# Kernel tuning notes

Measured on AMD Instinct MI355X. Metric: run time of the kernel, lower is better.

The kernel has to match this reference:

```python
import jax, jax.numpy as jnp
import numpy as np

B, SE, SD, IN_DIM, D, DEPTH, H, DH, M, FF, NBINS = 8, 2048, 1024, 1280, 512, 4, 8, 64, 266, 2048, 128

def _ln(x, g, b):
    mu = x.mean(-1, keepdims=True)
    var = ((x - mu) ** 2).mean(-1, keepdims=True)
    return (x - mu) / jnp.sqrt(var + 1e-5) * g + b

def _gelu(x):
    return jax.nn.gelu(x, approximate=False)

def _sinusoidal(x, dim):
    # sinusoidal embedding of integer expression bins -> [.., dim]
    half = dim // 2
    freqs = jnp.exp(-jnp.log(10000.0) * jnp.arange(half, dtype=jnp.float32) / half)
    ang = x[..., None].astype(jnp.float32) * freqs
    return jnp.concatenate([jnp.sin(ang), jnp.cos(ang)], axis=-1)

def _split_heads(x):
    b, s, _ = x.shape
    return x.reshape(b, s, H, DH).transpose(0, 2, 1, 3)

def _merge_heads(x):
    b, h, s, d = x.shape
    return x.transpose(0, 2, 1, 3).reshape(b, s, h * d)

def _favor_attention(q, k, v, proj):
    # FAVOR+ softmax-kernel linear attention (non-causal), performer-style
    dn = DH ** -0.25
    ratio = M ** -0.5
    eps = 1e-4
    qd = jnp.einsum('bhsd,md->bhsm', q * dn, proj)
    kd = jnp.einsum('bhsd,md->bhsm', k * dn, proj)
    q_diag = 0.5 * (q ** 2).sum(-1, keepdims=True) * dn * dn
    k_diag = 0.5 * (k ** 2).sum(-1, keepdims=True) * dn * dn
    qp = ratio * (jnp.exp(qd - q_diag - jnp.max(qd, axis=-1, keepdims=True)) + eps)
    kp = ratio * (jnp.exp(kd - k_diag - jnp.max(kd)) + eps)
    k_sum = kp.sum(axis=2)                                   # [b,h,m]
    d_inv = 1.0 / jnp.einsum('bhsm,bhm->bhs', qp, k_sum)     # [b,h,s]
    kv = jnp.einsum('bhsm,bhsd->bhmd', kp, v)                # [b,h,m,d]
    return jnp.einsum('bhsm,bhmd->bhsd', qp, kv) * d_inv[..., None]

def _forward(var_input_encoder, var_input_decoder, var_W, var_b, enc_ln_g, enc_ln_b, dec_ln_g, dec_ln_b, p_ln1_g, p_ln1_b, p_Wq, p_Wk, p_Wv, p_Wo, p_bo, p_ln2_g, p_ln2_b, p_w1, p_b1, p_w2, p_b2, proj, ca_Wq, ca_Wk, ca_Wv, ca_Wo, ca_bo, cross_ln_g, cross_ln_b, ffd_w1, ffd_b1, ffd_w2, ffd_b2, out_ln_g, out_ln_b, head_W, head_b, expression_encoder):
    expr = _sinusoidal(expression_encoder, D)            # [B,SE,D]
    enc = var_input_encoder @ var_W + var_b              # [B,SE,D]
    dec = var_input_decoder @ var_W + var_b              # [B,SD,D]
    x = _ln(enc + expr, enc_ln_g, enc_ln_b)
    # Performer encoder: pre-LN self-attn (FAVOR+) + pre-LN FF, residuals
    for i in range(DEPTH):
        y = _ln(x, p_ln1_g[i], p_ln1_b[i])
        q = _split_heads(y @ p_Wq[i])
        k = _split_heads(y @ p_Wk[i])
        v = _split_heads(y @ p_Wv[i])
        x = x + (_merge_heads(_favor_attention(q, k, v, proj[i])) @ p_Wo[i] + p_bo[i])
        y = _ln(x, p_ln2_g[i], p_ln2_b[i])
        x = x + (_gelu(y @ p_w1[i] + p_b1[i]) @ p_w2[i] + p_b2[i])
    context = x
    # decoder: LN -> softmax cross-attention over encoder context
    dec = _ln(dec, dec_ln_g, dec_ln_b)
    q = _split_heads(dec @ ca_Wq)
    k = _split_heads(context @ ca_Wk)
    v = _split_heads(context @ ca_Wv)
    scores = jnp.einsum('bhqd,bhkd->bhqk', q, k) * (DH ** -0.5)
    o = _merge_heads(jnp.einsum('bhqk,bhkd->bhqd', jax.nn.softmax(scores, axis=-1), v)) @ ca_Wo + ca_bo
    out = _ln(o + dec, cross_ln_g, cross_ln_b)
    out = _gelu(out @ ffd_w1 + ffd_b1) @ ffd_w2 + ffd_b2   # note: no residual around FF (as in source)
    out = _ln(out, out_ln_g, out_ln_b)
    return out @ head_W + head_b                            # [B,SD,NBINS]

def setup_inputs() -> dict:
    key = jax.random.key(0)
    ks = iter(jax.random.split(key, 64))
    def w(shape, scale=0.02):
        return jax.random.normal(next(ks), shape, dtype=jnp.float32) * scale
    inp = {
        'var_input_encoder': jax.random.normal(next(ks), (B, SE, IN_DIM), dtype=jnp.float32),
        'var_input_decoder': jax.random.normal(next(ks), (B, SD, IN_DIM), dtype=jnp.float32),
        'expression_encoder': jax.random.randint(next(ks), (B, SE), 0, NBINS, dtype=jnp.int32),
        'var_W': w((IN_DIM, D)), 'var_b': jnp.zeros((D,), jnp.float32),
        'enc_ln_g': jnp.ones((D,), jnp.float32), 'enc_ln_b': jnp.zeros((D,), jnp.float32),
        'dec_ln_g': jnp.ones((D,), jnp.float32), 'dec_ln_b': jnp.zeros((D,), jnp.float32),
        'p_ln1_g': jnp.ones((DEPTH, D), jnp.float32), 'p_ln1_b': jnp.zeros((DEPTH, D), jnp.float32),
        'p_Wq': w((DEPTH, D, H * DH)), 'p_Wk': w((DEPTH, D, H * DH)), 'p_Wv': w((DEPTH, D, H * DH)),
        'p_Wo': w((DEPTH, H * DH, D)), 'p_bo': jnp.zeros((DEPTH, D), jnp.float32),
        'p_ln2_g': jnp.ones((DEPTH, D), jnp.float32), 'p_ln2_b': jnp.zeros((DEPTH, D), jnp.float32),
        'p_w1': w((DEPTH, D, FF)), 'p_b1': jnp.zeros((DEPTH, FF), jnp.float32),
        'p_w2': w((DEPTH, FF, D)), 'p_b2': jnp.zeros((DEPTH, D), jnp.float32),
        'proj': jax.random.normal(next(ks), (DEPTH, M, DH), dtype=jnp.float32),
        'ca_Wq': w((D, H * DH)), 'ca_Wk': w((D, H * DH)), 'ca_Wv': w((D, H * DH)),
        'ca_Wo': w((H * DH, D)), 'ca_bo': jnp.zeros((D,), jnp.float32),
        'cross_ln_g': jnp.ones((D,), jnp.float32), 'cross_ln_b': jnp.zeros((D,), jnp.float32),
        'ffd_w1': w((D, FF)), 'ffd_b1': jnp.zeros((FF,), jnp.float32),
        'ffd_w2': w((FF, D)), 'ffd_b2': jnp.zeros((D,), jnp.float32),
        'out_ln_g': jnp.ones((D,), jnp.float32), 'out_ln_b': jnp.zeros((D,), jnp.float32),
        'head_W': w((D, NBINS)), 'head_b': jnp.zeros((NBINS,), jnp.float32),
    }
    return inp

def reference(var_input_encoder, var_input_decoder, expression_encoder, var_W, var_b, enc_ln_g, enc_ln_b, dec_ln_g, dec_ln_b, p_ln1_g, p_ln1_b, p_Wq, p_Wk, p_Wv, p_Wo, p_bo, p_ln2_g, p_ln2_b, p_w1, p_b1, p_w2, p_b2, proj, ca_Wq, ca_Wk, ca_Wv, ca_Wo, ca_bo, cross_ln_g, cross_ln_b, ffd_w1, ffd_b1, ffd_w2, ffd_b2, out_ln_g, out_ln_b, head_W, head_b):
    return _forward(var_input_encoder, var_input_decoder, var_W, var_b, enc_ln_g, enc_ln_b, dec_ln_g, dec_ln_b, p_ln1_g, p_ln1_b, p_Wq, p_Wk, p_Wv, p_Wo, p_bo, p_ln2_g, p_ln2_b, p_w1, p_b1, p_w2, p_b2, proj, ca_Wq, ca_Wk, ca_Wv, ca_Wo, ca_bo, cross_ln_g, cross_ln_b, ffd_w1, ffd_b1, ffd_w2, ffd_b2, out_ln_g, out_ln_b, head_W, head_b, expression_encoder)
```

## Files before the change

### kernel.cpp

```cpp
#include <hip/hip_runtime.h>
#include <hip/hip_bf16.h>
#include <math.h>

constexpr int cB = 8, cSE = 2048, cSD = 1024, cIN = 1280, cD = 512,
              cDEPTH = 4, cH = 8, cDH = 64, cM = 266, cFF = 2048, cNB = 128;
constexpr int cMP = 288;

#define DEV __device__ __forceinline__

typedef __bf16 bf16;
typedef __attribute__((ext_vector_type(8))) __bf16 bf16x8;
typedef __attribute__((ext_vector_type(4))) __bf16 bf16x4;
typedef __attribute__((ext_vector_type(2))) __bf16 bf16x2;
typedef __attribute__((ext_vector_type(4))) float f32x4;

DEV float gelu_f(float x) { return 0.5f * x * (1.0f + erff(x * 0.70710678118654752440f)); }

DEV float wave_sum(float v) {
#pragma unroll
  for (int o = 32; o; o >>= 1) v += __shfl_xor(v, o);
  return v;
}
DEV float wave_max(float v) {
#pragma unroll
  for (int o = 32; o; o >>= 1) v = fmaxf(v, __shfl_xor(v, o));
  return v;
}

#define GL2LDS(gp, lp) __builtin_amdgcn_global_load_lds(                    \
    (const __attribute__((address_space(1))) void*)(gp),                    \
    (__attribute__((address_space(3))) void*)(lp), 16, 0, 0)

template <int OUT, int ACT, bool BIAS, bool RES>
__global__ __launch_bounds__(256) void gemm_mfma(
    const bf16* __restrict__ A, const bf16* __restrict__ Bt,
    void* __restrict__ Cv, bf16* __restrict__ Cv2,
    const float* __restrict__ bias, int M, int N, int K) {
  __shared__ bf16 As[128 * 32];
  __shared__ bf16 Bs[128 * 32];
  const int t = threadIdx.x, l = t & 63, w = t >> 6;
  const int g = l >> 4, c = l & 15;
  const int nwg = gridDim.x * gridDim.y;
  int id = blockIdx.y * gridDim.x + blockIdx.x;
  if ((nwg & 7) == 0) id = (id & 7) * (nwg >> 3) + (id >> 3);
  const int m0 = (id / gridDim.x) * 128, n0 = (id % gridDim.x) * 128;
  const int wr = (w >> 1) * 64, wc = (w & 1) * 64;
  const int srow = w * 32 + (l >> 2);
  const int scol = (l & 3) * 8;
  const bf16* gA = A + (size_t)(m0 + srow) * K + scol;
  const bf16* gB = Bt + (size_t)(n0 + srow) * K + scol;
  bf16* lA = As + w * 1024;
  bf16* lB = Bs + w * 1024;

  const f32x4 zero4 = {0.f, 0.f, 0.f, 0.f};
  f32x4 acc[4][4];
#pragma unroll
  for (int i = 0; i < 4; i++)
#pragma unroll
    for (int j = 0; j < 4; j++) acc[i][j] = zero4;

  for (int k0 = 0; k0 < K; k0 += 32) {
    GL2LDS(gA + k0, lA);
    GL2LDS(gA + (size_t)16 * K + k0, lA + 512);
    GL2LDS(gB + k0, lB);
    GL2LDS(gB + (size_t)16 * K + k0, lB + 512);
    __syncthreads();
    bf16x8 af[4], bfr[4];
#pragma unroll
    for (int i = 0; i < 4; i++)
      af[i] = *(const bf16x8*)(As + (wr + i * 16 + c) * 32 + g * 8);
#pragma unroll
    for (int j = 0; j < 4; j++)
      bfr[j] = *(const bf16x8*)(Bs + (wc + j * 16 + c) * 32 + g * 8);
#pragma unroll
    for (int i = 0; i < 4; i++)
#pragma unroll
      for (int j = 0; j < 4; j++)
        acc[i][j] = __builtin_amdgcn_mfma_f32_16x16x32_bf16(af[i], bfr[j], acc[i][j], 0, 0, 0);
    __syncthreads();
  }
  float* Cf = (float*)Cv;
  bf16* Cb = (bf16*)Cv;
#pragma unroll
  for (int i = 0; i < 4; i++) {
    const int mb = m0 + wr + i * 16 + g * 4;
#pragma unroll
    for (int j = 0; j < 4; j++) {
      const int n = n0 + wc + j * 16 + c;
      const float bv = BIAS ? bias[n] : 0.f;
#pragma unroll
      for (int r = 0; r < 4; r++) {
        float v = acc[i][j][r] + bv;
        if (ACT == 1) v = gelu_f(v);
        const size_t idx = (size_t)(mb + r) * N + n;
        if (OUT == 0 || OUT == 2) {
          float* cp = Cf + idx;
          if (RES) v += *cp;
          *cp = v;
          if (OUT == 2) Cv2[idx] = (bf16)v;
        } else {
          Cb[idx] = (bf16)v;
        }
      }
    }
  }
}

__global__ __launch_bounds__(256) void transpose_cast(
    const float* __restrict__ W, bf16* __restrict__ Wt, int K, int N) {
  __shared__ float tile[32][33];
  const int tx = threadIdx.x & 31, ty = threadIdx.x >> 5;
  const int k0 = blockIdx.y * 32, n0 = blockIdx.x * 32;
#pragma unroll
  for (int i = ty; i < 32; i += 8) tile[i][tx] = W[(size_t)(k0 + i) * N + n0 + tx];
  __syncthreads();
#pragma unroll
  for (int i = ty; i < 32; i += 8)
    Wt[(size_t)(n0 + i) * K + k0 + tx] = (bf16)tile[tx][i];
}

__global__ __launch_bounds__(256) void transpose_cast4(
    const float* __restrict__ W0, const float* __restrict__ W1,
    const float* __restrict__ W2, const float* __restrict__ W3,
    bf16* __restrict__ Wt) {
  __shared__ float tile[32][33];
  const int zz = blockIdx.z;
  const float* W = zz == 0 ? W0 : zz == 1 ? W1 : zz == 2 ? W2 : W3;
  bf16* dst = Wt + (size_t)zz * 262144;
  const int tx = threadIdx.x & 31, ty = threadIdx.x >> 5;
  const int k0 = blockIdx.y * 32, n0 = blockIdx.x * 32;
#pragma unroll
  for (int i = ty; i < 32; i += 8) tile[i][tx] = W[(size_t)(k0 + i) * 512 + n0 + tx];
  __syncthreads();
#pragma unroll
  for (int i = ty; i < 32; i += 8)
    dst[(size_t)(n0 + i) * 512 + k0 + tx] = (bf16)tile[tx][i];
}

__global__ __launch_bounds__(256) void transpose_castFF(
    const float* __restrict__ w1s, const float* __restrict__ w2s,
    bf16* __restrict__ d1, bf16* __restrict__ d2) {
  __shared__ float tile[32][33];
  const int z = blockIdx.y;
  const int K = z ? 2048 : 512, N = z ? 512 : 2048;
  const float* W = z ? w2s : w1s;
  bf16* dst = z ? d2 : d1;
  const int nt = N >> 5;
  const int bid = blockIdx.x;
  const int n0 = (bid % nt) * 32, k0 = (bid / nt) * 32;
  const int tx = threadIdx.x & 31, ty = threadIdx.x >> 5;
#pragma unroll
  for (int i = ty; i < 32; i += 8) tile[i][tx] = W[(size_t)(k0 + i) * N + n0 + tx];
  __syncthreads();
#pragma unroll
  for (int i = ty; i < 32; i += 8)
    dst[(size_t)(n0 + i) * K + k0 + tx] = (bf16)tile[tx][i];
}

__global__ __launch_bounds__(256) void castf2b(
    const float* __restrict__ x, bf16* __restrict__ y, int n) {
  int i = (blockIdx.x * 256 + threadIdx.x) * 4;
  const int stride = gridDim.x * 1024;
  for (; i < n; i += stride) {
    float4 v = *(const float4*)(x + i);
    bf16x4 o;
    o[0] = (bf16)v.x; o[1] = (bf16)v.y; o[2] = (bf16)v.z; o[3] = (bf16)v.w;
    *(bf16x4*)(y + i) = o;
  }
}

__global__ __launch_bounds__(256) void proj_cast(
    const float* __restrict__ proj, bf16* __restrict__ projB) {
  const int idx = blockIdx.x * 256 + threadIdx.x;
  if (idx >= cMP * cDH) return;
  const int m = idx >> 6;
  projB[idx] = (bf16)(m < cM ? proj[idx] * 0.35355339059327373f : 0.f);
}

__global__ __launch_bounds__(256) void vtrans(
    const bf16* __restrict__ Vh, int ld, bf16* __restrict__ Vt) {
  __shared__ bf16 tile[64][65];
  const int z = blockIdx.y, b = z >> 3, h = z & 7;
  const int s0 = blockIdx.x * 64;
  const int t = threadIdx.x;
#pragma unroll
  for (int r = t >> 3; r < 64; r += 32) {
    bf16x8 v = *(const bf16x8*)(Vh + ((size_t)b * cSE + s0 + r) * ld + h * cDH + (t & 7) * 8);
#pragma unroll
    for (int e = 0; e < 8; e++) tile[(t & 7) * 8 + e][r] = v[e];
  }
  __syncthreads();
  bf16* vz = Vt + (size_t)z * 80 * cSE;
#pragma unroll
  for (int d = t >> 3; d < 64; d += 32) {
    bf16x8 o;
#pragma unroll
    for (int e = 0; e < 8; e++) o[e] = tile[d][(t & 7) * 8 + e];
    *(bf16x8*)(vz + (size_t)d * cSE + s0 + (t & 7) * 8) = o;
  }
  const int rr = t >> 4, seg = (t & 15) * 4;
  bf16x4 ov;
  const float val = (rr == 0) ? 1.f : 0.f;
  ov[0] = (bf16)val; ov[1] = (bf16)val; ov[2] = (bf16)val; ov[3] = (bf16)val;
  *(bf16x4*)(vz + (size_t)(64 + rr) * cSE + s0 + seg) = ov;
}

template <int MODE>
__global__ __launch_bounds__(256, 1) void favor_phik(
    const bf16* __restrict__ Kh, int ld, const bf16* __restrict__ projB,
    float* __restrict__ bmax, bf16* __restrict__ Pout) {
  __shared__ float sm[4];
  const int z = blockIdx.y, b = z >> 3, h = z & 7;
  const int s0 = blockIdx.x * 128;
  const int t = threadIdx.x, l = t & 63, w = t >> 6, g = l >> 4, c = l & 15;
  const int wr = (w >> 1) * 64, wcol = (w & 1) * 144;

  float gm = 0.f;
  if (MODE == 2) {
    float m = -1e30f;
    for (int i = t; i < 1024; i += 256) m = fmaxf(m, bmax[i]);
    m = wave_max(m);
    if (l == 0) sm[w] = m;
    __syncthreads();
    gm = fmaxf(fmaxf(sm[0], sm[1]), fmaxf(sm[2], sm[3]));
  }

  const f32x4 zero4 = {0.f, 0.f, 0.f, 0.f};
  f32x4 acc[4][9];
#pragma unroll
  for (int i = 0; i < 4; i++)
#pragma unroll
    for (int j = 0; j < 9; j++) acc[i][j] = zero4;
  float sq[4] = {0.f, 0.f, 0.f, 0.f};
  const size_t abase = ((size_t)b * cSE + s0) * ld + h * cDH;
#pragma unroll
  for (int k0 = 0; k0 < 64; k0 += 32) {
    bf16x8 af[4];
#pragma unroll
    for (int i = 0; i < 4; i++) {
      af[i] = *(const bf16x8*)(Kh + abase + (size_t)(wr + i * 16 + c) * ld + k0 + g * 8);
      if (MODE == 2) {
#pragma unroll
        for (int e = 0; e < 8; e++) {
          const float v = (float)af[i][e];
          sq[i] += v * v;
        }
      }
    }
#pragma unroll
    for (int j = 0; j < 9; j++) {
      bf16x8 bfr = *(const bf16x8*)(projB + (wcol + j * 16 + c) * 64 + k0 + g * 8);
#pragma unroll
      for (int i = 0; i < 4; i++)
        acc[i][j] = __builtin_amdgcn_mfma_f32_16x16x32_bf16(af[i], bfr, acc[i][j], 0, 0, 0);
    }
  }
  const float ratio = 0.061313927f;

  if (MODE == 1) {
    float m = -3e38f;
#pragma unroll
    for (int i = 0; i < 4; i++)
#pragma unroll
      for (int j = 0; j < 9; j++) {
        const int mc = wcol + j * 16 + c;
        if (mc < cM) {
#pragma unroll
          for (int r = 0; r < 4; r++) m = fmaxf(m, acc[i][j][r]);
        }
      }
    m = wave_max(m);
    if (l == 0) sm[w] = m;
    __syncthreads();
    if (t == 0)
      bmax[blockIdx.y * 16 + blockIdx.x] =
          fmaxf(fmaxf(sm[0], sm[1]), fmaxf(sm[2], sm[3]));
    return;
  }

#pragma unroll
  for (int i = 0; i < 4; i++) {
    sq[i] += __shfl_xor(sq[i], 16);
    sq[i] += __shfl_xor(sq[i], 32);
  }
  float rowsub[4][4];
#pragma unroll
  for (int i = 0; i < 4; i++)
#pragma unroll
    for (int r = 0; r < 4; r++)
      rowsub[i][r] = gm + 0.0625f * __shfl(sq[i], g * 4 + r);

#pragma unroll
  for (int i = 0; i < 4; i++)
#pragma unroll
    for (int j = 0; j < 9; j++) {
      const int mc = wcol + j * 16 + c;
      bf16x4 o;
#pragma unroll
      for (int r = 0; r < 4; r++) {
        const float v = (mc < cM)
            ? ratio * (__expf(acc[i][j][r] - rowsub[i][r]) + 1e-4f) : 0.f;
        o[r] = (bf16)v;
      }
      *(bf16x4*)(Pout + ((size_t)z * cMP + mc) * cSE + s0 + wr + i * 16 + g * 4) = o;
    }
}

__global__ __launch_bounds__(256) void favor_kv(
    const bf16* __restrict__ Pk, const bf16* __restrict__ Vt,
    float* __restrict__ part) {
  const int z = blockIdx.y, ch = blockIdx.x;
  const int t = threadIdx.x, l = t & 63, w = t >> 6, g = l >> 4, c = l & 15;
  const int wm = (w & 1) * 144, wd = (w >> 1) * 32;
  const bool dden = (wd == 32);
  const size_t pkz = (size_t)z * cMP * cSE, vtz = (size_t)z * 80 * cSE;
  const f32x4 zero4 = {0.f, 0.f, 0.f, 0.f};
  f32x4 acc[9][2], accx[9];
#pragma unroll
  for (int j = 0; j < 9; j++) {
    acc[j][0] = zero4; acc[j][1] = zero4; accx[j] = zero4;
  }
  for (int k0 = ch * 512; k0 < ch * 512 + 512; k0 += 32) {
    bf16x8 bv[2], bvx;
#pragma unroll
    for (int i = 0; i < 2; i++)
      bv[i] = *(const bf16x8*)(Vt + vtz + (size_t)(wd + i * 16 + c) * cSE + k0 + g * 8);
    if (dden)
      bvx = *(const bf16x8*)(Vt + vtz + (size_t)(64 + c) * cSE + k0 + g * 8);
#pragma unroll
    for (int j = 0; j < 9; j++) {
      bf16x8 am = *(const bf16x8*)(Pk + pkz + (size_t)(wm + j * 16 + c) * cSE + k0 + g * 8);
      acc[j][0] = __builtin_amdgcn_mfma_f32_16x16x32_bf16(am, bv[0], acc[j][0], 0, 0, 0);
      acc[j][1] = __builtin_amdgcn_mfma_f32_16x16x32_bf16(am, bv[1], acc[j][1], 0, 0, 0);
      if (dden)
        accx[j] = __builtin_amdgcn_mfma_f32_16x16x32_bf16(am, bvx, accx[j], 0, 0, 0);
    }
  }
  float* po = part + ((size_t)z * 4 + ch) * (cMP * 80);
#pragma unroll
  for (int j = 0; j < 9; j++)
#pragma unroll
    for (int i = 0; i < 2; i++)
#pragma unroll
      for (int r = 0; r < 4; r++)
        po[(size_t)(wm + j * 16 + g * 4 + r) * 80 + wd + i * 16 + c] = acc[j][i][r];
  if (dden) {
#pragma unroll
    for (int j = 0; j < 9; j++)
#pragma unroll
      for (int r = 0; r < 4; r++)
        po[(size_t)(wm + j * 16 + g * 4 + r) * 80 + 64 + c] = accx[j][r];
  }
}

__global__ __launch_bounds__(256) void kv_reduce(
    const float* __restrict__ part, bf16* __restrict__ kvT) {
  const int z = blockIdx.x;
  const float* p = part + (size_t)z * 4 * (cMP * 80);
  bf16* o = kvT + (size_t)z * 80 * cMP;
  for (int idx = threadIdx.x; idx < cMP * 80; idx += 256) {
    const int m = idx / 80, d = idx - m * 80;
    const float s = p[idx] + p[idx + cMP * 80] + p[idx + 2 * cMP * 80] + p[idx + 3 * cMP * 80];
    o[(size_t)d * cMP + m] = (bf16)s;
  }
}

__global__ __launch_bounds__(256, 1) void favor_qout(
    const bf16* __restrict__ Qh, int ld, const bf16* __restrict__ projB,
    const bf16* __restrict__ kvT, bf16* __restrict__ Y) {
  __shared__ bf16 Plds[128 * 296];
  __shared__ float rmaxs[4][64];
  __shared__ float denl[128];
  const int z = blockIdx.y, b = z >> 3, h = z & 7;
  const int s0 = blockIdx.x * 128;
  const int t = threadIdx.x, l = t & 63, w = t >> 6, g = l >> 4, c = l & 15;
  const int wr = (w >> 1) * 64, wcol = (w & 1) * 144;
  const f32x4 zero4 = {0.f, 0.f, 0.f, 0.f};
  f32x4 acc[4][9];
#pragma unroll
  for (int i = 0; i < 4; i++)
#pragma unroll
    for (int j = 0; j < 9; j++) acc[i][j] = zero4;
  float sq[4] = {0.f, 0.f, 0.f, 0.f};
  const size_t abase = ((size_t)b * cSE + s0) * ld + h * cDH;
#pragma unroll
  for (int k0 = 0; k0 < 64; k0 += 32) {
    bf16x8 af[4];
#pragma unroll
    for (int i = 0; i < 4; i++) {
      af[i] = *(const bf16x8*)(Qh + abase + (size_t)(wr + i * 16 + c) * ld + k0 + g * 8);
#pragma unroll
      for (int e = 0; e < 8; e++) {
        const float v = (float)af[i][e];
        sq[i] += v * v;
      }
    }
#pragma unroll
    for (int j = 0; j < 9; j++) {
      bf16x8 bfr = *(const bf16x8*)(projB + (wcol + j * 16 + c) * 64 + k0 + g * 8);
#pragma unroll
      for (int i = 0; i < 4; i++)
        acc[i][j] = __builtin_amdgcn_mfma_f32_16x16x32_bf16(af[i], bfr, acc[i][j], 0, 0, 0);
    }
  }
#pragma unroll
  for (int i = 0; i < 4; i++) {
    sq[i] += __shfl_xor(sq[i], 16);
    sq[i] += __shfl_xor(sq[i], 32);
  }
  const float ratio = 0.061313927f;
  float rowsub[4][4];
#pragma unroll
  for (int i = 0; i < 4; i++)
#pragma unroll
    for (int r = 0; r < 4; r++) {
      float m = -3e38f;
#pragma unroll
      for (int j = 0; j < 9; j++) {
        const int mc = wcol + j * 16 + c;
        m = (mc < cM) ? fmaxf(m, acc[i][j][r]) : m;
      }
      m = fmaxf(m, __shfl_xor(m, 1));
      m = fmaxf(m, __shfl_xor(m, 2));
      m = fmaxf(m, __shfl_xor(m, 4));
      m = fmaxf(m, __shfl_xor(m, 8));
      rowsub[i][r] = m;
    }
  if (c == 0) {
#pragma unroll
    for (int i = 0; i < 4; i++)
#pragma unroll
      for (int r = 0; r < 4; r++) rmaxs[w][i * 16 + g * 4 + r] = rowsub[i][r];
  }
  __syncthreads();
#pragma unroll
  for (int i = 0; i < 4; i++)
#pragma unroll
    for (int r = 0; r < 4; r++) {
      const int row = i * 16 + g * 4 + r;
      rowsub[i][r] = fmaxf(rowsub[i][r], rmaxs[w ^ 1][row]) +
                     0.0625f * __shfl(sq[i], g * 4 + r);
    }
#pragma unroll
  for (int i = 0; i < 4; i++)
#pragma unroll
    for (int j = 0; j < 9; j++) {
      const int mc = wcol + j * 16 + c;
#pragma unroll
      for (int r = 0; r < 4; r++) {
        const float v = (mc < cM)
            ? ratio * (__expf(acc[i][j][r] - rowsub[i][r]) + 1e-4f) : 0.f;
        Plds[(wr + i * 16 + g * 4 + r) * 296 + mc] = (bf16)v;
      }
    }
  __syncthreads();

  const int wd = (w & 1) * 32;
  const bool dden = (wd == 32);
  f32x4 acc2[4][2], accx[4];
#pragma unroll
  for (int i = 0; i < 4; i++) {
    acc2[i][0] = zero4; acc2[i][1] = zero4; accx[i] = zero4;
  }
  const size_t kz = (size_t)z * 80 * cMP;
#pragma unroll 3
  for (int k0 = 0; k0 < cMP; k0 += 32) {
    bf16x8 bv[2], bvx;
#pragma unroll
    for (int j = 0; j < 2; j++)
      bv[j] = *(const bf16x8*)(kvT + kz + (size_t)(wd + j * 16 + c) * cMP + k0 + g * 8);
    if (dden)
      bvx = *(const bf16x8*)(kvT + kz + (size_t)(64 + c) * cMP + k0 + g * 8);
#pragma unroll
    for (int i = 0; i < 4; i++) {
      bf16x8 av = *(const bf16x8*)(Plds + (wr + i * 16 + c) * 296 + k0 + g * 8);
      acc2[i][0] = __builtin_amdgcn_mfma_f32_16x16x32_bf16(av, bv[0], acc2[i][0], 0, 0, 0);
      acc2[i][1] = __builtin_amdgcn_mfma_f32_16x16x32_bf16(av, bv[1], acc2[i][1], 0, 0, 0);
      if (dden)
        accx[i] = __builtin_amdgcn_mfma_f32_16x16x32_bf16(av, bvx, accx[i], 0, 0, 0);
    }
  }
  if (dden && c == 0) {
#pragma unroll
    for (int i = 0; i < 4; i++)
#pragma unroll
      for (int r = 0; r < 4; r++)
        denl[wr + i * 16 + g * 4 + r] = accx[i][r];
  }
  __syncthreads();
#pragma unroll
  for (int i = 0; i < 4; i++)
#pragma unroll
    for (int r = 0; r < 4; r++) {
      const int row = wr + i * 16 + g * 4 + r;
      const float inv = 1.0f / denl[row];
#pragma unroll
      for (int j = 0; j < 2; j++)
        Y[((size_t)b * cSE + s0 + row) * cD + h * cDH + wd + j * 16 + c] =
            (bf16)(acc2[i][j][r] * inv);
    }
}

template <bool ADD, bool WF, bool WB>
__global__ __launch_bounds__(256) void ln_rows(
    const float* __restrict__ in, const float* __restrict__ add,
    const float* __restrict__ g, const float* __restrict__ be,
    float* __restrict__ out, bf16* __restrict__ out2) {
  const int wid = blockIdx.x * 4 + (threadIdx.x >> 6);
  const int lane = threadIdx.x & 63;
  const float* ip = in + (size_t)wid * cD + lane * 8;
  float x[8];
  {
    float4 a = *(const float4*)ip;
    float4 b4 = *(const float4*)(ip + 4);
    x[0] = a.x; x[1] = a.y; x[2] = a.z; x[3] = a.w;
    x[4] = b4.x; x[5] = b4.y; x[6] = b4.z; x[7] = b4.w;
  }
  if (ADD) {
    const float* ap = add + (size_t)wid * cD + lane * 8;
    float4 a = *(const float4*)ap;
    float4 b4 = *(const float4*)(ap + 4);
    x[0] += a.x; x[1] += a.y; x[2] += a.z; x[3] += a.w;
    x[4] += b4.x; x[5] += b4.y; x[6] += b4.z; x[7] += b4.w;
  }
  float s = 0;
#pragma unroll
  for (int i = 0; i < 8; i++) s += x[i];
  s = wave_sum(s);
  const float mu = s * (1.0f / cD);
  float vs = 0;
#pragma unroll
  for (int i = 0; i < 8; i++) { const float d = x[i] - mu; vs += d * d; }
  vs = wave_sum(vs);
  const float rstd = 1.0f / sqrtf(vs * (1.0f / cD) + 1e-5f);
  float r[8];
#pragma unroll
  for (int i = 0; i < 8; i++) {
    const int d = lane * 8 + i;
    r[i] = (x[i] - mu) * rstd * g[d] + be[d];
  }
  if (WF) {
    float* op = out + (size_t)wid * cD + lane * 8;
    float4 a, b4;
    a.x = r[0]; a.y = r[1]; a.z = r[2]; a.w = r[3];
    b4.x = r[4]; b4.y = r[5]; b4.z = r[6]; b4.w = r[7];
    *(float4*)op = a; *(float4*)(op + 4) = b4;
  }
  if (WB) {
    bf16x8 ov;
#pragma unroll
    for (int i = 0; i < 8; i++) ov[i] = (bf16)r[i];
    *(bf16x8*)(out2 + (size_t)wid * cD + lane * 8) = ov;
  }
}

__global__ __launch_bounds__(256) void embed_ln(
    float* __restrict__ X, const int* __restrict__ ids,
    const float* __restrict__ g, const float* __restrict__ be) {
  const int wid = blockIdx.x * 4 + (threadIdx.x >> 6);
  const int lane = threadIdx.x & 63;
  const float idv = (float)ids[wid];
  float* xp = X + (size_t)wid * cD + lane * 8;
  float x[8];
  {
    float4 a = *(const float4*)xp;
    float4 b4 = *(const float4*)(xp + 4);
    x[0] = a.x; x[1] = a.y; x[2] = a.z; x[3] = a.w;
    x[4] = b4.x; x[5] = b4.y; x[6] = b4.z; x[7] = b4.w;
  }
  const float kf = -0.03597789207803197f;
#pragma unroll
  for (int i = 0; i < 8; i++) {
    const int d = lane * 8 + i;
    float e;
    if (d < 256) e = sinf(idv * expf(kf * (float)d));
    else         e = cosf(idv * expf(kf * (float)(d - 256)));
    x[i] += e;
  }
  float s = 0;
#pragma unroll
  for (int i = 0; i < 8; i++) s += x[i];
  s = wave_sum(s);
  const float mu = s * (1.0f / cD);
  float vs = 0;
#pragma unroll
  for (int i = 0; i < 8; i++) { const float d = x[i] - mu; vs += d * d; }
  vs = wave_sum(vs);
  const float rstd = 1.0f / sqrtf(vs * (1.0f / cD) + 1e-5f);
#pragma unroll
  for (int i = 0; i < 8; i++) {
    const int d = lane * 8 + i;
    xp[i] = (x[i] - mu) * rstd * g[d] + be[d];
  }
}

__global__ __launch_bounds__(256) void flash_mfma(
    const bf16* __restrict__ Q, const bf16* __restrict__ Kc,
    const bf16* __restrict__ Vc, bf16* __restrict__ O, int ldkv) {
  __shared__ __align__(16) bf16 KP[4 * 16 * 136];
  __shared__ __align__(16) bf16 Vs[80 * 136];
  const int id = blockIdx.x;
  const int b = (id & 63) >> 3, h = id & 7, qb = id >> 6;
  const int t = threadIdx.x, l = t & 63, w = t >> 6, g = l >> 4, c = l & 15;
  const int q0 = qb * 64 + w * 16;
  bf16x8 aq[2];
  {
    const bf16* qp = Q + ((size_t)b * cSD + q0 + c) * cD + h * cDH + g * 8;
    aq[0] = *(const bf16x8*)qp;
    aq[1] = *(const bf16x8*)(qp + 32);
  }
  for (int idx = t; idx < 16 * 136; idx += 256) {
    const int rr = idx / 136, cc = idx - rr * 136;
    Vs[(64 + rr) * 136 + cc] = (bf16)(rr == 0 ? 1.f : 0.f);
  }
  const f32x4 zero4 = {0.f, 0.f, 0.f, 0.f};
  f32x4 o5[5];
#pragma unroll
  for (int j = 0; j < 5; j++) o5[j] = zero4;
  float mrow[4];
#pragma unroll
  for (int r = 0; r < 4; r++) mrow[r] = -1e30f;

  const int kr = t >> 1, kof = (t & 1) * 32;
  const int sidx = t & 31, dseg = t >> 5;
  const size_t kvbase = (size_t)b * cSE * ldkv + h * cDH;
  char* KsC = (char*)KP;
  bf16* Pw = KP + w * 16 * 136;
  const float S2 = 0.18033688011112042f;
  const float T2 = 11.541560327111708f;

  bf16x8 pk[4], pv[4];
  auto LOADR = [&](int kt) {
    const bf16* kp = Kc + kvbase + (size_t)(kt + kr) * ldkv + kof;
#pragma unroll
    for (int i = 0; i < 4; i++) pk[i] = *(const bf16x8*)(kp + i * 8);
    const bf16* vp = Vc + kvbase + (size_t)(kt + 4 * sidx) * ldkv + dseg * 8;
#pragma unroll
    for (int i = 0; i < 4; i++) pv[i] = *(const bf16x8*)(vp + (size_t)i * ldkv);
  };
  auto WRITEL = [&]() {
    const int sw = (kr & 7) << 4;
#pragma unroll
    for (int i = 0; i < 4; i++)
      *(bf16x8*)(KsC + kr * 128 + (((kof + i * 8) * 2) ^ sw)) = pk[i];
#pragma unroll
    for (int e = 0; e < 8; e++) {
      bf16x4 q4;
      q4[0] = pv[0][e]; q4[1] = pv[1][e]; q4[2] = pv[2][e]; q4[3] = pv[3][e];
      *(bf16x4*)(Vs + (dseg * 8 + e) * 136 + 4 * sidx) = q4;
    }
  };
  LOADR(0);
  WRITEL();

  for (int kt = 0; kt < cSE; kt += 128) {
    const bool more = (kt + 128 < cSE);
    if (more) LOADR(kt + 128);
    __syncthreads();
    f32x4 s4[8];
#pragma unroll
    for (int t2 = 0; t2 < 8; t2++) {
      const int kr2 = t2 * 16 + c;
      const int sw2 = (kr2 & 7) << 4;
      bf16x8 bk0 = *(const bf16x8*)(KsC + kr2 * 128 + ((g * 16) ^ sw2));
      bf16x8 bk1 = *(const bf16x8*)(KsC + kr2 * 128 + ((64 + g * 16) ^ sw2));
      f32x4 z = zero4;
      z = __builtin_amdgcn_mfma_f32_16x16x32_bf16(aq[0], bk0, z, 0, 0, 0);
      z = __builtin_amdgcn_mfma_f32_16x16x32_bf16(aq[1], bk1, z, 0, 0, 0);
      s4[t2] = z;
    }
    __syncthreads();
#pragma unroll
    for (int r = 0; r < 4; r++) {
      float xv[8];
#pragma unroll
      for (int t2 = 0; t2 < 8; t2++) xv[t2] = s4[t2][r] * S2;
      float tm = xv[0];
#pragma unroll
      for (int t2 = 1; t2 < 8; t2++) tm = fmaxf(tm, xv[t2]);
      tm = fmaxf(tm, __shfl_xor(tm, 1));
      tm = fmaxf(tm, __shfl_xor(tm, 2));
      tm = fmaxf(tm, __shfl_xor(tm, 4));
      tm = fmaxf(tm, __shfl_xor(tm, 8));
      if (tm > mrow[r] + T2) {
        const float corr = exp2f(mrow[r] - tm);
        mrow[r] = tm;
#pragma unroll
        for (int j = 0; j < 5; j++) o5[j][r] *= corr;
      }
      const float m = mrow[r];
      const int qr = g * 4 + r;
#pragma unroll
      for (int t2 = 0; t2 < 8; t2++)
        Pw[qr * 136 + t2 * 16 + c] = (bf16)exp2f(xv[t2] - m);
    }
    bf16x8 pa[4];
#pragma unroll
    for (int ks = 0; ks < 4; ks++)
      pa[ks] = *(const bf16x8*)(Pw + c * 136 + ks * 32 + g * 8);
#pragma unroll
    for (int j = 0; j < 5; j++) {
#pragma unroll
      for (int ks = 0; ks < 4; ks++) {
        bf16x8 bv = *(const bf16x8*)(Vs + (j * 16 + c) * 136 + ks * 32 + g * 8);
        o5[j] = __builtin_amdgcn_mfma_f32_16x16x32_bf16(pa[ks], bv, o5[j], 0, 0, 0);
      }
    }
    __syncthreads();
    if (more) WRITEL();
  }
#pragma unroll
  for (int r = 0; r < 4; r++) {
    const float den = __shfl(o5[4][r], l & 48);
    const float inv = 1.0f / den;
    const size_t row = (size_t)b * cSD + q0 + g * 4 + r;
#pragma unroll
    for (int j = 0; j < 4; j++)
      O[row * cD + h * cDH + j * 16 + c] = (bf16)(o5[j][r] * inv);
  }
}

extern "C" void kernel_launch(void* const* d_in, const int* in_sizes, int n_in,
                              void* d_out, int out_size, void* d_ws, size_t ws_size,
                              hipStream_t stream) {
  const float* in_enc = (const float*)d_in[0];
  const float* in_dec = (const float*)d_in[1];
  const int* expr = (const int*)d_in[2];
  const float* var_W = (const float*)d_in[3];
  const float* var_b = (const float*)d_in[4];
  const float* enc_g = (const float*)d_in[5];
  const float* enc_b = (const float*)d_in[6];
  const float* dec_g = (const float*)d_in[7];
  const float* dec_b = (const float*)d_in[8];
  const float* ln1_g = (const float*)d_in[9];
  const float* ln1_b = (const float*)d_in[10];
  const float* Wq = (const float*)d_in[11];
  const float* Wk = (const float*)d_in[12];
  const float* Wv = (const float*)d_in[13];
  const float* Wo = (const float*)d_in[14];
  const float* bo = (const float*)d_in[15];
  const float* ln2_g = (const float*)d_in[16];
  const float* ln2_b = (const float*)d_in[17];
  const float* w1 = (const float*)d_in[18];
  const float* b1 = (const float*)d_in[19];
  const float* w2 = (const float*)d_in[20];
  const float* b2 = (const float*)d_in[21];
  const float* proj = (const float*)d_in[22];
  const float* caWq = (const float*)d_in[23];
  const float* caWk = (const float*)d_in[24];
  const float* caWv = (const float*)d_in[25];
  const float* caWo = (const float*)d_in[26];
  const float* cabo = (const float*)d_in[27];
  const float* crg = (const float*)d_in[28];
  const float* crb = (const float*)d_in[29];
  const float* fw1 = (const float*)d_in[30];
  const float* fb1 = (const float*)d_in[31];
  const float* fw2 = (const float*)d_in[32];
  const float* fb2 = (const float*)d_in[33];
  const float* og = (const float*)d_in[34];
  const float* ob = (const float*)d_in[35];
  const float* hW = (const float*)d_in[36];
  const float* hb = (const float*)d_in[37];

  float* X     = (float*)d_ws;
  float* DC    = X + 8388608;
  bf16*  QKV   = (bf16*)(DC + 4194304);
  bf16*  Vt    = QKV + 25165824;
  bf16*  Pq    = Vt + 10485760;
  bf16*  Pk    = Pq + 37748736;
  float* part  = (float*)(Pk + 37748736);
  bf16*  kvT   = (bf16*)(part + 5898240);
  float* bmax  = (float*)(kvT + 1474560);
  bf16*  Yb    = (bf16*)(bmax + 1040);
  bf16*  DCb   = Yb + 8388608;
  bf16*  Wt    = DCb + 4194304;
  bf16*  projB = Wt + 1048576;
  bf16*  Wt2   = projB + 18432;
  const size_t need_bytes = (size_t)82143264 * 4;
  if (ws_size < need_bytes) return;

  bf16* Pb   = Pq;
  bf16* encB = Pb;
  bf16* decB = Pk;
  bf16* Pmid = Pb;
  bf16* Xb   = Vt;
  bf16* Qc   = Pb + 8388608;
  bf16* KVc  = Pb + 12582912;
  bf16* Fb   = Pb + 29360128;
  bf16* Pm2  = Pb + 33554432;

  const dim3 blk(256);

  castf2b<<<2048, blk, 0, stream>>>(in_enc, encB, 16384 * 1280);
  castf2b<<<2048, blk, 0, stream>>>(in_dec, decB, 8192 * 1280);
  transpose_cast<<<dim3(16, 40), blk, 0, stream>>>(var_W, Wt, 1280, 512);
  gemm_mfma<0, 0, true, false><<<dim3(4, 128), blk, 0, stream>>>(encB, Wt, X, nullptr, var_b, 16384, 512, 1280);
  gemm_mfma<0, 0, true, false><<<dim3(4, 64), blk, 0, stream>>>(decB, Wt, DC, nullptr, var_b, 8192, 512, 1280);
  embed_ln<<<4096, blk, 0, stream>>>(X, expr, enc_g, enc_b);
  ln_rows<false, true, true><<<2048, blk, 0, stream>>>(DC, nullptr, dec_g, dec_b, DC, DCb);

  for (int i = 0; i < cDEPTH; i++) {
    ln_rows<false, false, true><<<4096, blk, 0, stream>>>(X, nullptr, ln1_g + i * cD, ln1_b + i * cD, nullptr, Yb);
    transpose_cast4<<<dim3(16, 16, 4), blk, 0, stream>>>(
        Wq + (size_t)i * cD * cD, Wk + (size_t)i * cD * cD,
        Wv + (size_t)i * cD * cD, Wo + (size_t)i * cD * cD, Wt);
    gemm_mfma<1, 0, false, false><<<dim3(12, 128), blk, 0, stream>>>(Yb, Wt, QKV, nullptr, nullptr, 16384, 1536, 512);
    proj_cast<<<72, blk, 0, stream>>>(proj + (size_t)i * cM * cDH, projB);
    vtrans<<<dim3(32, 64), blk, 0, stream>>>(QKV + 1024, 1536, Vt);
    favor_phik<1><<<dim3(16, 64), blk, 0, stream>>>(QKV + 512, 1536, projB, bmax, nullptr);
    favor_phik<2><<<dim3(16, 64), blk, 0, stream>>>(QKV + 512, 1536, projB, bmax, Pk);
    favor_kv<<<dim3(4, 64), blk, 0, stream>>>(Pk, Vt, part);
    kv_reduce<<<64, blk, 0, stream>>>(part, kvT);
    favor_qout<<<dim3(16, 64), blk, 0, stream>>>(QKV, 1536, projB, kvT, Yb);
    gemm_mfma<0, 0, true, true><<<dim3(4, 128), blk, 0, stream>>>(Yb, Wt + 786432, X, nullptr, bo + i * cD, 16384, 512, 512);
    ln_rows<false, false, true><<<4096, blk, 0, stream>>>(X, nullptr, ln2_g + i * cD, ln2_b + i * cD, nullptr, Yb);
    transpose_castFF<<<dim3(1024, 2), blk, 0, stream>>>(
        w1 + (size_t)i * cD * cFF, w2 + (size_t)i * cFF * cD, Wt, Wt2);
    gemm_mfma<1, 1, true, false><<<dim3(16, 128), blk, 0, stream>>>(Yb, Wt, Pmid, nullptr, b1 + i * cFF, 16384, 2048, 512);
    if (i < cDEPTH - 1) {
      gemm_mfma<0, 0, true, true><<<dim3(4, 128), blk, 0, stream>>>(Pmid, Wt2, X, nullptr, b2 + i * cD, 16384, 512, 2048);
    } else {
      gemm_mfma<2, 0, true, true><<<dim3(4, 128), blk, 0, stream>>>(Pmid, Wt2, X, Xb, b2 + i * cD, 16384, 512, 2048);
    }
  }

  transpose_cast4<<<dim3(16, 16, 4), blk, 0, stream>>>(caWq, caWk, caWv, caWo, Wt);
  gemm_mfma<1, 0, false, false><<<dim3(4, 64), blk, 0, stream>>>(DCb, Wt, Qc, nullptr, nullptr, 8192, 512, 512);
  gemm_mfma<1, 0, false, false><<<dim3(8, 128), blk, 0, stream>>>(Xb, Wt + 262144, KVc, nullptr, nullptr, 16384, 1024, 512);
  flash_mfma<<<dim3(1024), blk, 0, stream>>>(Qc, KVc, KVc + 512, Fb, 1024);
  gemm_mfma<0, 0, true, false><<<dim3(4, 64), blk, 0, stream>>>(Fb, Wt + 786432, X, nullptr, cabo, 8192, 512, 512);
  ln_rows<true, false, true><<<2048, blk, 0, stream>>>(X, DC, crg, crb, nullptr, Yb);
  transpose_castFF<<<dim3(1024, 2), blk, 0, stream>>>(fw1, fw2, Wt, Wt2);
  gemm_mfma<1, 1, true, false><<<dim3(16, 64), blk, 0, stream>>>(Yb, Wt, Pm2, nullptr, fb1, 8192, 2048, 512);
  gemm_mfma<0, 0, true, false><<<dim3(4, 64), blk, 0, stream>>>(Pm2, Wt2, X + 4194304, nullptr, fb2, 8192, 512, 2048);
  ln_rows<false, false, true><<<2048, blk, 0, stream>>>(X + 4194304, nullptr, og, ob, nullptr, Yb);
  transpose_cast<<<dim3(4, 16), blk, 0, stream>>>(hW, Wt, 512, 128);
  gemm_mfma<0, 0, true, false><<<dim3(1, 64), blk, 0, stream>>>(Yb, Wt, (float*)d_out, nullptr, hb, 8192, 128, 512);
}
```

Baseline: 2.276 ms.

## Fuse FAVOR key feature map with KV accumulation via shared memory

Merges the second key feature-map pass and the KV contraction into a single kernel. Each block computes exp feature tiles for 64 keys into LDS and immediately multiplies them with V, so the large Pk buffer is never written to or read from global memory. The work is split into 8 sequence chunks instead of 4, and kv_reduce now sums 8 partials. Separately, the softmax scale of the cross-attention query is folded into the Q projection GEMM epilogue, removing a multiply in the flash loop. The fused kernel keeps many accumulators live, which adds register pressure, and it needs extra block barriers.

```diff
diff --git a/kernel.cpp b/kernel.cpp
--- a/kernel.cpp
+++ b/kernel.cpp
@@ -92,6 +92,7 @@
       for (int r = 0; r < 4; r++) {
         float v = acc[i][j][r] + bv;
         if (ACT == 1) v = gelu_f(v);
+        if (ACT == 2) v *= 0.18033688011112042f;
         const size_t idx = (size_t)(mb + r) * N + n;
         if (OUT == 0 || OUT == 2) {
           float* cp = Cf + idx;
@@ -205,18 +206,65 @@
   *(bf16x4*)(vz + (size_t)(64 + rr) * cSE + s0 + seg) = ov;
 }
 
-template <int MODE>
-__global__ __launch_bounds__(256, 1) void favor_phik(
+__global__ __launch_bounds__(256, 1) void favor_kmax(
     const bf16* __restrict__ Kh, int ld, const bf16* __restrict__ projB,
-    float* __restrict__ bmax, bf16* __restrict__ Pout) {
+    float* __restrict__ bmax) {
   __shared__ float sm[4];
   const int z = blockIdx.y, b = z >> 3, h = z & 7;
   const int s0 = blockIdx.x * 128;
   const int t = threadIdx.x, l = t & 63, w = t >> 6, g = l >> 4, c = l & 15;
   const int wr = (w >> 1) * 64, wcol = (w & 1) * 144;
-
-  float gm = 0.f;
-  if (MODE == 2) {
+  const f32x4 zero4 = {0.f, 0.f, 0.f, 0.f};
+  f32x4 acc[4][9];
+#pragma unroll
+  for (int i = 0; i < 4; i++)
+#pragma unroll
+    for (int j = 0; j < 9; j++) acc[i][j] = zero4;
+  const size_t abase = ((size_t)b * cSE + s0) * ld + h * cDH;
+#pragma unroll
+  for (int k0 = 0; k0 < 64; k0 += 32) {
+    bf16x8 af[4];
+#pragma unroll
+    for (int i = 0; i < 4; i++)
+      af[i] = *(const bf16x8*)(Kh + abase + (size_t)(wr + i * 16 + c) * ld + k0 + g * 8);
+#pragma unroll
+    for (int j = 0; j < 9; j++) {
+      bf16x8 bfr = *(const bf16x8*)(projB + (wcol + j * 16 + c) * 64 + k0 + g * 8);
+#pragma unroll
+      for (int i = 0; i < 4; i++)
+        acc[i][j] = __builtin_amdgcn_mfma_f32_16x16x32_bf16(af[i], bfr, acc[i][j], 0, 0, 0);
+    }
+  }
+  float m = -3e38f;
+#pragma unroll
+  for (int i = 0; i < 4; i++)
+#pragma unroll
+    for (int j = 0; j < 9; j++) {
+      const int mc = wcol + j * 16 + c;
+      if (mc < cM) {
+#pragma unroll
+        for (int r = 0; r < 4; r++) m = fmaxf(m, acc[i][j][r]);
+      }
+    }
+  m = wave_max(m);
+  if (l == 0) sm[w] = m;
+  __syncthreads();
+  if (t == 0)
+    bmax[blockIdx.y * 16 + blockIdx.x] =
+        fmaxf(fmaxf(sm[0], sm[1]), fmaxf(sm[2], sm[3]));
+}
+
+__global__ __launch_bounds__(256, 1) void favor_kkv(
+    const bf16* __restrict__ Kh, int ld, const bf16* __restrict__ projB,
+    const bf16* __restrict__ Vt, const float* __restrict__ bmax,
+    float* __restrict__ part) {
+  __shared__ bf16 kp[288 * 72];
+  __shared__ float sm[4];
+  const int z = blockIdx.y, b = z >> 3, h = z & 7;
+  const int chunk = blockIdx.x;
+  const int t = threadIdx.x, l = t & 63, w = t >> 6, g = l >> 4, c = l & 15;
+  float gm;
+  {
     float m = -1e30f;
     for (int i = t; i < 1024; i += 256) m = fmaxf(m, bmax[i]);
     m = wave_max(m);
@@ -224,143 +272,118 @@
     __syncthreads();
     gm = fmaxf(fmaxf(sm[0], sm[1]), fmaxf(sm[2], sm[3]));
   }
-
+  const int pr = (w >> 1) * 32;
+  const int wcol = (w & 1) * 144;
+  const int wm = (w & 1) * 144, wd = (w >> 1) * 32;
+  const bool dden = (wd == 32);
+  const float ratio = 0.061313927f;
   const f32x4 zero4 = {0.f, 0.f, 0.f, 0.f};
-  f32x4 acc[4][9];
-#pragma unroll
-  for (int i = 0; i < 4; i++)
-#pragma unroll
-    for (int j = 0; j < 9; j++) acc[i][j] = zero4;
-  float sq[4] = {0.f, 0.f, 0.f, 0.f};
-  const size_t abase = ((size_t)b * cSE + s0) * ld + h * cDH;
-#pragma unroll
-  for (int k0 = 0; k0 < 64; k0 += 32) {
-    bf16x8 af[4];
-#pragma unroll
-    for (int i = 0; i < 4; i++) {
-      af[i] = *(const bf16x8*)(Kh + abase + (size_t)(wr + i * 16 + c) * ld + k0 + g * 8);
-      if (MODE == 2) {
+  f32x4 kacc[9][2], kaccx[9];
+#pragma unroll
+  for (int j = 0; j < 9; j++) {
+    kacc[j][0] = zero4; kacc[j][1] = zero4; kaccx[j] = zero4;
+  }
+  const size_t kbase = (size_t)b * cSE * ld + h * cDH;
+  const size_t vtz = (size_t)z * 80 * cSE;
+
+  for (int st = 0; st < 256; st += 64) {
+    const int sg = chunk * 256 + st;
+    f32x4 pacc[2][9];
+#pragma unroll
+    for (int i = 0; i < 2; i++)
+#pragma unroll
+      for (int j = 0; j < 9; j++) pacc[i][j] = zero4;
+    float sq[2] = {0.f, 0.f};
+#pragma unroll
+    for (int k0 = 0; k0 < 64; k0 += 32) {
+      bf16x8 af[2];
+#pragma unroll
+      for (int i = 0; i < 2; i++) {
+        af[i] = *(const bf16x8*)(Kh + kbase + (size_t)(sg + pr + i * 16 + c) * ld + k0 + g * 8);
 #pragma unroll
         for (int e = 0; e < 8; e++) {
           const float v = (float)af[i][e];
           sq[i] += v * v;
         }
       }
-    }
-#pragma unroll
-    for (int j = 0; j < 9; j++) {
-      bf16x8 bfr = *(const bf16x8*)(projB + (wcol + j * 16 + c) * 64 + k0 + g * 8);
-#pragma unroll
-      for (int i = 0; i < 4; i++)
-        acc[i][j] = __builtin_amdgcn_mfma_f32_16x16x32_bf16(af[i], bfr, acc[i][j], 0, 0, 0);
-    }
-  }
-  const float ratio = 0.061313927f;
-
-  if (MODE == 1) {
-    float m = -3e38f;
-#pragma unroll
-    for (int i = 0; i < 4; i++)
+#pragma unroll
+      for (int j = 0; j < 9; j++) {
+        bf16x8 bfr = *(const bf16x8*)(projB + (wcol + j * 16 + c) * 64 + k0 + g * 8);
+        pacc[0][j] = __builtin_amdgcn_mfma_f32_16x16x32_bf16(af[0], bfr, pacc[0][j], 0, 0, 0);
+        pacc[1][j] = __builtin_amdgcn_mfma_f32_16x16x32_bf16(af[1], bfr, pacc[1][j], 0, 0, 0);
+      }
+    }
+#pragma unroll
+    for (int i = 0; i < 2; i++) {
+      sq[i] += __shfl_xor(sq[i], 16);
+      sq[i] += __shfl_xor(sq[i], 32);
+    }
+    float rowsub[2][4];
+#pragma unroll
+    for (int i = 0; i < 2; i++)
+#pragma unroll
+      for (int r = 0; r < 4; r++)
+        rowsub[i][r] = gm + 0.0625f * __shfl(sq[i], g * 4 + r);
+    __syncthreads();
+#pragma unroll
+    for (int i = 0; i < 2; i++)
 #pragma unroll
       for (int j = 0; j < 9; j++) {
         const int mc = wcol + j * 16 + c;
-        if (mc < cM) {
-#pragma unroll
-          for (int r = 0; r < 4; r++) m = fmaxf(m, acc[i][j][r]);
+        bf16x4 o;
+#pragma unroll
+        for (int r = 0; r < 4; r++) {
+          const float v = (mc < cM)
+              ? ratio * (__expf(pacc[i][j][r] - rowsub[i][r]) + 1e-4f) : 0.f;
+          o[r] = (bf16)v;
         }
-      }
-    m = wave_max(m);
-    if (l == 0) sm[w] = m;
+        *(bf16x4*)(kp + (size_t)mc * 72 + pr + i * 16 + g * 4) = o;
+      }
     __syncthreads();
-    if (t == 0)
-      bmax[blockIdx.y * 16 + blockIdx.x] =
-          fmaxf(fmaxf(sm[0], sm[1]), fmaxf(sm[2], sm[3]));
-    return;
-  }
-
-#pragma unroll
-  for (int i = 0; i < 4; i++) {
-    sq[i] += __shfl_xor(sq[i], 16);
-    sq[i] += __shfl_xor(sq[i], 32);
-  }
-  float rowsub[4][4];
-#pragma unroll
-  for (int i = 0; i < 4; i++)
-#pragma unroll
-    for (int r = 0; r < 4; r++)
-      rowsub[i][r] = gm + 0.0625f * __shfl(sq[i], g * 4 + r);
-
-#pragma unroll
-  for (int i = 0; i < 4; i++)
-#pragma unroll
-    for (int j = 0; j < 9; j++) {
-      const int mc = wcol + j * 16 + c;
-      bf16x4 o;
-#pragma unroll
-      for (int r = 0; r < 4; r++) {
-        const float v = (mc < cM)
-            ? ratio * (__expf(acc[i][j][r] - rowsub[i][r]) + 1e-4f) : 0.f;
-        o[r] = (bf16)v;
-      }
-      *(bf16x4*)(Pout + ((size_t)z * cMP + mc) * cSE + s0 + wr + i * 16 + g * 4) = o;
-    }
-}
-
-__global__ __launch_bounds__(256) void favor_kv(
-    const bf16* __restrict__ Pk, const bf16* __restrict__ Vt,
-    float* __restrict__ part) {
-  const int z = blockIdx.y, ch = blockIdx.x;
-  const int t = threadIdx.x, l = t & 63, w = t >> 6, g = l >> 4, c = l & 15;
-  const int wm = (w & 1) * 144, wd = (w >> 1) * 32;
-  const bool dden = (wd == 32);
-  const size_t pkz = (size_t)z * cMP * cSE, vtz = (size_t)z * 80 * cSE;
-  const f32x4 zero4 = {0.f, 0.f, 0.f, 0.f};
-  f32x4 acc[9][2], accx[9];
-#pragma unroll
-  for (int j = 0; j < 9; j++) {
-    acc[j][0] = zero4; acc[j][1] = zero4; accx[j] = zero4;
-  }
-  for (int k0 = ch * 512; k0 < ch * 512 + 512; k0 += 32) {
-    bf16x8 bv[2], bvx;
+#pragma unroll
+    for (int k0 = 0; k0 < 64; k0 += 32) {
+      bf16x8 bv0 = *(const bf16x8*)(Vt + vtz + (size_t)(wd + c) * cSE + sg + k0 + g * 8);
+      bf16x8 bv1 = *(const bf16x8*)(Vt + vtz + (size_t)(wd + 16 + c) * cSE + sg + k0 + g * 8);
+      bf16x8 bvx;
+      if (dden)
+        bvx = *(const bf16x8*)(Vt + vtz + (size_t)(64 + c) * cSE + sg + k0 + g * 8);
+#pragma unroll
+      for (int j = 0; j < 9; j++) {
+        bf16x8 am = *(const bf16x8*)(kp + (size_t)(wm + j * 16 + c) * 72 + k0 + g * 8);
+        kacc[j][0] = __builtin_amdgcn_mfma_f32_16x16x32_bf16(am, bv0, kacc[j][0], 0, 0, 0);
+        kacc[j][1] = __builtin_amdgcn_mfma_f32_16x16x32_bf16(am, bv1, kacc[j][1], 0, 0, 0);
+        if (dden)
+          kaccx[j] = __builtin_amdgcn_mfma_f32_16x16x32_bf16(am, bvx, kaccx[j], 0, 0, 0);
+      }
+    }
+  }
+  float* po = part + ((size_t)z * 8 + chunk) * (cMP * 80);
+#pragma unroll
+  for (int j = 0; j < 9; j++)
 #pragma unroll
     for (int i = 0; i < 2; i++)
-      bv[i] = *(const bf16x8*)(Vt + vtz + (size_t)(wd + i * 16 + c) * cSE + k0 + g * 8);
-    if (dden)
-      bvx = *(const bf16x8*)(Vt + vtz + (size_t)(64 + c) * cSE + k0 + g * 8);
-#pragma unroll
-    for (int j = 0; j < 9; j++) {
-      bf16x8 am = *(const bf16x8*)(Pk + pkz + (size_t)(wm + j * 16 + c) * cSE + k0 + g * 8);
-      acc[j][0] = __builtin_amdgcn_mfma_f32_16x16x32_bf16(am, bv[0], acc[j][0], 0, 0, 0);
-      acc[j][1] = __builtin_amdgcn_mfma_f32_16x16x32_bf16(am, bv[1], acc[j][1], 0, 0, 0);
-      if (dden)
-        accx[j] = __builtin_amdgcn_mfma_f32_16x16x32_bf16(am, bvx, accx[j], 0, 0, 0);
-    }
-  }
-  float* po = part + ((size_t)z * 4 + ch) * (cMP * 80);
-#pragma unroll
-  for (int j = 0; j < 9; j++)
-#pragma unroll
-    for (int i = 0; i < 2; i++)
 #pragma unroll
       for (int r = 0; r < 4; r++)
-        po[(size_t)(wm + j * 16 + g * 4 + r) * 80 + wd + i * 16 + c] = acc[j][i][r];
+        po[(size_t)(wm + j * 16 + g * 4 + r) * 80 + wd + i * 16 + c] = kacc[j][i][r];
   if (dden) {
 #pragma unroll
     for (int j = 0; j < 9; j++)
 #pragma unroll
       for (int r = 0; r < 4; r++)
-        po[(size_t)(wm + j * 16 + g * 4 + r) * 80 + 64 + c] = accx[j][r];
+        po[(size_t)(wm + j * 16 + g * 4 + r) * 80 + 64 + c] = kaccx[j][r];
   }
 }
 
 __global__ __launch_bounds__(256) void kv_reduce(
     const float* __restrict__ part, bf16* __restrict__ kvT) {
   const int z = blockIdx.x;
-  const float* p = part + (size_t)z * 4 * (cMP * 80);
+  const float* p = part + (size_t)z * 8 * (cMP * 80);
   bf16* o = kvT + (size_t)z * 80 * cMP;
   for (int idx = threadIdx.x; idx < cMP * 80; idx += 256) {
     const int m = idx / 80, d = idx - m * 80;
-    const float s = p[idx] + p[idx + cMP * 80] + p[idx + 2 * cMP * 80] + p[idx + 3 * cMP * 80];
+    float s = 0.f;
+#pragma unroll
+    for (int cc = 0; cc < 8; cc++) s += p[idx + (size_t)cc * (cMP * 80)];
     o[(size_t)d * cMP + m] = (bf16)s;
   }
 }
@@ -626,7 +649,6 @@
   const size_t kvbase = (size_t)b * cSE * ldkv + h * cDH;
   char* KsC = (char*)KP;
   bf16* Pw = KP + w * 16 * 136;
-  const float S2 = 0.18033688011112042f;
   const float T2 = 11.541560327111708f;
 
   bf16x8 pk[4], pv[4];
@@ -674,7 +696,7 @@
     for (int r = 0; r < 4; r++) {
       float xv[8];
 #pragma unroll
-      for (int t2 = 0; t2 < 8; t2++) xv[t2] = s4[t2][r] * S2;
+      for (int t2 = 0; t2 < 8; t2++) xv[t2] = s4[t2][r];
       float tm = xv[0];
 #pragma unroll
       for (int t2 = 1; t2 < 8; t2++) tm = fmaxf(tm, xv[t2]);
@@ -766,22 +788,20 @@
   float* DC    = X + 8388608;
   bf16*  QKV   = (bf16*)(DC + 4194304);
   bf16*  Vt    = QKV + 25165824;
-  bf16*  Pq    = Vt + 10485760;
-  bf16*  Pk    = Pq + 37748736;
-  float* part  = (float*)(Pk + 37748736);
-  bf16*  kvT   = (bf16*)(part + 5898240);
+  bf16*  Pb    = Vt + 10485760;
+  float* part  = (float*)(Pb + 50331648);
+  bf16*  kvT   = (bf16*)(part + 11796480);
   float* bmax  = (float*)(kvT + 1474560);
   bf16*  Yb    = (bf16*)(bmax + 1040);
   bf16*  DCb   = Yb + 8388608;
   bf16*  Wt    = DCb + 4194304;
   bf16*  projB = Wt + 1048576;
   bf16*  Wt2   = projB + 18432;
-  const size_t need_bytes = (size_t)82143264 * 4;
+  const size_t need_bytes = (size_t)75458576 * 4;
   if (ws_size < need_bytes) return;
 
-  bf16* Pb   = Pq;
   bf16* encB = Pb;
-  bf16* decB = Pk;
+  bf16* decB = (bf16*)part;
   bf16* Pmid = Pb;
   bf16* Xb   = Vt;
   bf16* Qc   = Pb + 8388608;
@@ -807,9 +827,8 @@
     gemm_mfma<1, 0, false, false><<<dim3(12, 128), blk, 0, stream>>>(Yb, Wt, QKV, nullptr, nullptr, 16384, 1536, 512);
     proj_cast<<<72, blk, 0, stream>>>(proj + (size_t)i * cM * cDH, projB);
     vtrans<<<dim3(32, 64), blk, 0, stream>>>(QKV + 1024, 1536, Vt);
-    favor_phik<1><<<dim3(16, 64), blk, 0, stream>>>(QKV + 512, 1536, projB, bmax, nullptr);
-    favor_phik<2><<<dim3(16, 64), blk, 0, stream>>>(QKV + 512, 1536, projB, bmax, Pk);
-    favor_kv<<<dim3(4, 64), blk, 0, stream>>>(Pk, Vt, part);
+    favor_kmax<<<dim3(16, 64), blk, 0, stream>>>(QKV + 512, 1536, projB, bmax);
+    favor_kkv<<<dim3(8, 64), blk, 0, stream>>>(QKV + 512, 1536, projB, Vt, bmax, part);
     kv_reduce<<<64, blk, 0, stream>>>(part, kvT);
     favor_qout<<<dim3(16, 64), blk, 0, stream>>>(QKV, 1536, projB, kvT, Yb);
     gemm_mfma<0, 0, true, true><<<dim3(4, 128), blk, 0, stream>>>(Yb, Wt + 786432, X, nullptr, bo + i * cD, 16384, 512, 512);
@@ -825,7 +844,7 @@
   }
 
   transpose_cast4<<<dim3(16, 16, 4), blk, 0, stream>>>(caWq, caWk, caWv, caWo, Wt);
-  gemm_mfma<1, 0, false, false><<<dim3(4, 64), blk, 0, stream>>>(DCb, Wt, Qc, nullptr, nullptr, 8192, 512, 512);
+  gemm_mfma<1, 2, false, false><<<dim3(4, 64), blk, 0, stream>>>(DCb, Wt, Qc, nullptr, nullptr, 8192, 512, 512);
   gemm_mfma<1, 0, false, false><<<dim3(8, 128), blk, 0, stream>>>(Xb, Wt + 262144, KVc, nullptr, nullptr, 16384, 1024, 512);
   flash_mfma<<<dim3(1024), blk, 0, stream>>>(Qc, KVc, KVc + 512, Fb, 1024);
   gemm_mfma<0, 0, true, false><<<dim3(4, 64), blk, 0, stream>>>(Fb, Wt + 786432, X, nullptr, cabo, 8192, 512, 512);
```

New measurement: 2.044 ms. -10.2%, faster.
